# Kernel optimization log

Hardware: AMD Instinct MI355X
Metric: run time of the kernel (lower is better)

## Reference

```python
import jax, jax.numpy as jnp
import numpy as np

B, T, E, D, H = 8, 64, 4, 256, 1024  # batch, num_tokens, num_experts, hidden_dim, ffn_hidden_dim
SPARSITY_WEIGHT = 0.01


def setup_inputs() -> dict:
    key = jax.random.key(0)
    k_x, k_fc1, k_fc2, k_wr, k_br = jax.random.split(key, 5)
    x = jax.random.normal(k_x, (B, T, D), dtype=jnp.float32)
    # xavier_uniform per (t,e) slice: bound = sqrt(6/(fan_in+fan_out))
    a = float(np.sqrt(6.0 / (D + H)))
    fc1 = jax.random.uniform(k_fc1, (T, E, D, H), minval=-a, maxval=a, dtype=jnp.float32)
    b1 = jnp.zeros((T, E, H), dtype=jnp.float32)
    fc2 = jax.random.uniform(k_fc2, (T, E, H, D), minval=-a, maxval=a, dtype=jnp.float32)
    b2 = jnp.zeros((T, E, D), dtype=jnp.float32)
    # per-token routers (nn.Linear default init: U(-1/sqrt(D), 1/sqrt(D)))
    br_bound = float(1.0 / np.sqrt(D))
    Wr = jax.random.uniform(k_wr, (T, E, D), minval=-br_bound, maxval=br_bound, dtype=jnp.float32)
    br = jax.random.uniform(k_br, (T, E), minval=-br_bound, maxval=br_bound, dtype=jnp.float32)
    return {"x": x, "fc1": fc1, "b1": b1, "fc2": fc2, "b2": b2, "Wr": Wr, "br": br}


def reference(x, fc1, b1, fc2, b2, Wr, br):
    # x: [B,T,D]
    # ReLU routing gates per token/expert: [B,T,E]
    gates = jax.nn.relu(jnp.einsum('btd,ted->bte', x, Wr) + br)
    bsz = x.shape[0]
    aux_loss = SPARSITY_WEIGHT * gates.sum() / (bsz * x.shape[1])
    # Expert FFN, batched over (token, expert): hidden [B,T,E,H]
    hidden = jax.nn.gelu(jnp.einsum('btd,tedh->bteh', x, fc1) + b1, approximate=False)
    # dropout rate is 0.0 -> identity
    expert_out = jnp.einsum('bteh,tehd->bted', hidden, fc2) + b2  # [B,T,E,D]
    output = jnp.sum(expert_out * gates[..., None], axis=2)  # [B,T,D]
    return output, aux_loss
```

## Files before the change

kernel.cpp:

```cpp
#include <hip/hip_runtime.h>
#include <hip/hip_bf16.h>

namespace {

constexpr int kB = 8, kT = 64, kE = 4, kD = 256, kH = 1024;
constexpr int kNC = 4;
constexpr int kHc = kH / kNC;

typedef float floatx4 __attribute__((ext_vector_type(4)));

__device__ __forceinline__ float gelu_exact(float v) {
  return 0.5f * v * (1.0f + erff(v * 0.70710678118654752f));
}

__device__ __forceinline__ float4 ntload4(const float4* p) {
  const floatx4 v = __builtin_nontemporal_load(reinterpret_cast<const floatx4*>(p));
  return make_float4(v.x, v.y, v.z, v.w);
}

__global__ __launch_bounds__(256, 4)
void moe_ffn_kernel(const float* __restrict__ x,
                    const float* __restrict__ fc1,
                    const float* __restrict__ b1,
                    const float* __restrict__ fc2,
                    const float* __restrict__ b2,
                    const float* __restrict__ Wr,
                    const float* __restrict__ br,
                    float* __restrict__ out) {
  __shared__ float xs[kB][kD];
  __shared__ float hid[kB][kHc];
  __shared__ float red[kB][kD];
  __shared__ float gates_s[kB];

  const int tid  = threadIdx.x;
  const int bid  = blockIdx.x;
  const int te   = bid >> 2;
  const int c    = bid & 3;
  const int t    = te >> 2;
  const int h0   = c * kHc;
  const int wave = tid >> 6, lane = tid & 63;

  {
    const float4* __restrict__ xsrc = reinterpret_cast<const float4*>(x);
    float4* xdst = reinterpret_cast<float4*>(&xs[0][0]);
#pragma unroll
    for (int i = 0; i < 2; ++i) {
      const int f = i * 256 + tid;
      const int b = f >> 6, d4 = f & 63;
      xdst[f] = xsrc[(size_t)(b * kT + t) * (kD / 4) + d4];
    }
  }
  __syncthreads();

  {
    const float* __restrict__ wr = Wr + (size_t)te * kD;
    const float w0 = wr[lane], w1 = wr[lane + 64], w2 = wr[lane + 128], w3 = wr[lane + 192];
#pragma unroll
    for (int bb = 0; bb < 2; ++bb) {
      const int b = wave * 2 + bb;
      float p = xs[b][lane] * w0 + xs[b][lane + 64] * w1 +
                xs[b][lane + 128] * w2 + xs[b][lane + 192] * w3;
#pragma unroll
      for (int off = 32; off; off >>= 1) p += __shfl_xor(p, off);
      if (lane == 0) {
        const float g = p + br[te];
        gates_s[b] = g > 0.0f ? g : 0.0f;
      }
    }
  }

  float4 acc[kB];
#pragma unroll
  for (int b = 0; b < kB; ++b) acc[b] = make_float4(0.f, 0.f, 0.f, 0.f);
  {
    const float4* __restrict__ wp =
        reinterpret_cast<const float4*>(fc1 + (size_t)te * (kD * kH));
    const int hq = (h0 >> 2) + lane;
    const int d0 = wave * 64;
    for (int dg = 0; dg < 16; ++dg) {
      const int d = d0 + dg * 4;
      const float4 wv0 = wp[(size_t)(d + 0) * (kH / 4) + hq];
      const float4 wv1 = wp[(size_t)(d + 1) * (kH / 4) + hq];
      const float4 wv2 = wp[(size_t)(d + 2) * (kH / 4) + hq];
      const float4 wv3 = wp[(size_t)(d + 3) * (kH / 4) + hq];
#pragma unroll
      for (int b = 0; b < kB; ++b) {
        const float4 xv = *reinterpret_cast<const float4*>(&xs[b][d]);
        acc[b].x = fmaf(xv.x, wv0.x, acc[b].x);
        acc[b].y = fmaf(xv.x, wv0.y, acc[b].y);
        acc[b].z = fmaf(xv.x, wv0.z, acc[b].z);
        acc[b].w = fmaf(xv.x, wv0.w, acc[b].w);
        acc[b].x = fmaf(xv.y, wv1.x, acc[b].x);
        acc[b].y = fmaf(xv.y, wv1.y, acc[b].y);
        acc[b].z = fmaf(xv.y, wv1.z, acc[b].z);
        acc[b].w = fmaf(xv.y, wv1.w, acc[b].w);
        acc[b].x = fmaf(xv.z, wv2.x, acc[b].x);
        acc[b].y = fmaf(xv.z, wv2.y, acc[b].y);
        acc[b].z = fmaf(xv.z, wv2.z, acc[b].z);
        acc[b].w = fmaf(xv.z, wv2.w, acc[b].w);
        acc[b].x = fmaf(xv.w, wv3.x, acc[b].x);
        acc[b].y = fmaf(xv.w, wv3.y, acc[b].y);
        acc[b].z = fmaf(xv.w, wv3.z, acc[b].z);
        acc[b].w = fmaf(xv.w, wv3.w, acc[b].w);
      }
    }
  }
#pragma unroll
  for (int g = 0; g < 4; ++g) {
    if (wave == g) {
#pragma unroll
      for (int b = 0; b < kB; ++b) {
        float4* hp = reinterpret_cast<float4*>(&hid[b][0]) + lane;
        if (g == 0) {
          *hp = acc[b];
        } else {
          float4 v = *hp;
          v.x += acc[b].x; v.y += acc[b].y; v.z += acc[b].z; v.w += acc[b].w;
          *hp = v;
        }
      }
    }
    __syncthreads();
  }
  {
    const float bias = b1[(size_t)te * kH + h0 + tid];
#pragma unroll
    for (int b = 0; b < kB; ++b) hid[b][tid] = gelu_exact(hid[b][tid] + bias);
  }
  __syncthreads();

  float4 acc2[kB];
#pragma unroll
  for (int b = 0; b < kB; ++b) acc2[b] = make_float4(0.f, 0.f, 0.f, 0.f);
  {
    const float4* __restrict__ wp =
        reinterpret_cast<const float4*>(fc2 + (size_t)te * (kH * kD));
    const int hb = wave * 64;
    for (int hg = 0; hg < 16; ++hg) {
      const int hl = hb + hg * 4;
      const int h  = h0 + hl;
      const float4 wv0 = ntload4(wp + (size_t)(h + 0) * (kD / 4) + lane);
      const float4 wv1 = ntload4(wp + (size_t)(h + 1) * (kD / 4) + lane);
      const float4 wv2 = ntload4(wp + (size_t)(h + 2) * (kD / 4) + lane);
      const float4 wv3 = ntload4(wp + (size_t)(h + 3) * (kD / 4) + lane);
#pragma unroll
      for (int b = 0; b < kB; ++b) {
        const float4 hv = *reinterpret_cast<const float4*>(&hid[b][hl]);
        acc2[b].x = fmaf(hv.x, wv0.x, acc2[b].x);
        acc2[b].y = fmaf(hv.x, wv0.y, acc2[b].y);
        acc2[b].z = fmaf(hv.x, wv0.z, acc2[b].z);
        acc2[b].w = fmaf(hv.x, wv0.w, acc2[b].w);
        acc2[b].x = fmaf(hv.y, wv1.x, acc2[b].x);
        acc2[b].y = fmaf(hv.y, wv1.y, acc2[b].y);
        acc2[b].z = fmaf(hv.y, wv1.z, acc2[b].z);
        acc2[b].w = fmaf(hv.y, wv1.w, acc2[b].w);
        acc2[b].x = fmaf(hv.z, wv2.x, acc2[b].x);
        acc2[b].y = fmaf(hv.z, wv2.y, acc2[b].y);
        acc2[b].z = fmaf(hv.z, wv2.z, acc2[b].z);
        acc2[b].w = fmaf(hv.z, wv2.w, acc2[b].w);
        acc2[b].x = fmaf(hv.w, wv3.x, acc2[b].x);
        acc2[b].y = fmaf(hv.w, wv3.y, acc2[b].y);
        acc2[b].z = fmaf(hv.w, wv3.z, acc2[b].z);
        acc2[b].w = fmaf(hv.w, wv3.w, acc2[b].w);
      }
    }
  }
#pragma unroll
  for (int g = 0; g < 4; ++g) {
    if (wave == g) {
#pragma unroll
      for (int b = 0; b < kB; ++b) {
        float4* rp = reinterpret_cast<float4*>(&red[b][0]) + lane;
        if (g == 0) {
          *rp = acc2[b];
        } else {
          float4 v = *rp;
          v.x += acc2[b].x; v.y += acc2[b].y; v.z += acc2[b].z; v.w += acc2[b].w;
          *rp = v;
        }
      }
    }
    __syncthreads();
  }

  {
    const float b2v = (c == 0) ? b2[(size_t)te * kD + tid] : 0.f;
#pragma unroll
    for (int b = 0; b < kB; ++b)
      atomicAdd(&out[((size_t)b * kT + t) * kD + tid], gates_s[b] * (red[b][tid] + b2v));

    if (c == 0 && tid == 0) {
      float gs = 0.f;
#pragma unroll
      for (int b = 0; b < kB; ++b) gs += gates_s[b];
      atomicAdd(&out[(size_t)kB * kT * kD], 0.01f * gs * (1.0f / (kB * kT)));
    }
  }
}

}

extern "C" void kernel_launch(void* const* d_in, const int* in_sizes, int n_in,
                              void* d_out, int out_size, void* d_ws, size_t ws_size,
                              hipStream_t stream) {
  const float* x   = (const float*)d_in[0];
  const float* fc1 = (const float*)d_in[1];
  const float* b1  = (const float*)d_in[2];
  const float* fc2 = (const float*)d_in[3];
  const float* b2  = (const float*)d_in[4];
  const float* Wr  = (const float*)d_in[5];
  const float* br  = (const float*)d_in[6];
  float* out = (float*)d_out;

  (void)hipMemsetAsync(d_out, 0, (size_t)out_size * sizeof(float), stream);

  moe_ffn_kernel<<<dim3(kT * kE * kNC), dim3(256), 0, stream>>>(
      x, fc1, b1, fc2, b2, Wr, br, out);
}
```

Before: 95.89 us.

## Split hidden dim into eight chunks per expert and reuse xs for reduction

Doubles the number of H-chunks per (token, expert) to 2048 blocks, each handling 128 hidden units, to raise parallelism and occupancy (launch bounds raised to 8). The fc1 stage is remapped so half-waves cover different d rows and are combined with a cross-lane shuffle, and fc1 loads become nontemporal. The separate reduction buffer is dropped by reusing xs, which cuts shared memory per block. In exchange, output atomics double and the reduction and sync work per unit of compute grows.

```diff
diff --git a/kernel.cpp b/kernel.cpp
--- a/kernel.cpp
+++ b/kernel.cpp
@@ -4,7 +4,7 @@
 namespace {
 
 constexpr int kB = 8, kT = 64, kE = 4, kD = 256, kH = 1024;
-constexpr int kNC = 4;
+constexpr int kNC = 8;
 constexpr int kHc = kH / kNC;
 
 typedef float floatx4 __attribute__((ext_vector_type(4)));
@@ -18,7 +18,7 @@
   return make_float4(v.x, v.y, v.z, v.w);
 }
 
-__global__ __launch_bounds__(256, 4)
+__global__ __launch_bounds__(256, 8)
 void moe_ffn_kernel(const float* __restrict__ x,
                     const float* __restrict__ fc1,
                     const float* __restrict__ b1,
@@ -29,15 +29,13 @@
                     float* __restrict__ out) {
   __shared__ float xs[kB][kD];
   __shared__ float hid[kB][kHc];
-  __shared__ float red[kB][kD];
   __shared__ float gates_s[kB];
 
   const int tid  = threadIdx.x;
   const int bid  = blockIdx.x;
-  const int te   = bid >> 2;
-  const int c    = bid & 3;
+  const int te   = bid >> 3;
+  const int c    = bid & 7;
   const int t    = te >> 2;
-  const int h0   = c * kHc;
   const int wave = tid >> 6, lane = tid & 63;
 
   {
@@ -69,63 +67,72 @@
     }
   }
 
-  float4 acc[kB];
-#pragma unroll
-  for (int b = 0; b < kB; ++b) acc[b] = make_float4(0.f, 0.f, 0.f, 0.f);
+  const int q = lane & 31, r = lane >> 5;
+  const int hq = c * 32 + q;
+  float4 a[kB];
+#pragma unroll
+  for (int b = 0; b < kB; ++b) a[b] = make_float4(0.f, 0.f, 0.f, 0.f);
   {
     const float4* __restrict__ wp =
         reinterpret_cast<const float4*>(fc1 + (size_t)te * (kD * kH));
-    const int hq = (h0 >> 2) + lane;
     const int d0 = wave * 64;
+#pragma unroll 4
     for (int dg = 0; dg < 16; ++dg) {
-      const int d = d0 + dg * 4;
-      const float4 wv0 = wp[(size_t)(d + 0) * (kH / 4) + hq];
-      const float4 wv1 = wp[(size_t)(d + 1) * (kH / 4) + hq];
-      const float4 wv2 = wp[(size_t)(d + 2) * (kH / 4) + hq];
-      const float4 wv3 = wp[(size_t)(d + 3) * (kH / 4) + hq];
+      const int dbase = d0 + dg * 4;
+      const int row0 = dbase + r;
+      const int row1 = dbase + 2 + r;
+      const float4 wv0 = ntload4(wp + (size_t)row0 * (kH / 4) + hq);
+      const float4 wv1 = ntload4(wp + (size_t)row1 * (kH / 4) + hq);
 #pragma unroll
       for (int b = 0; b < kB; ++b) {
-        const float4 xv = *reinterpret_cast<const float4*>(&xs[b][d]);
-        acc[b].x = fmaf(xv.x, wv0.x, acc[b].x);
-        acc[b].y = fmaf(xv.x, wv0.y, acc[b].y);
-        acc[b].z = fmaf(xv.x, wv0.z, acc[b].z);
-        acc[b].w = fmaf(xv.x, wv0.w, acc[b].w);
-        acc[b].x = fmaf(xv.y, wv1.x, acc[b].x);
-        acc[b].y = fmaf(xv.y, wv1.y, acc[b].y);
-        acc[b].z = fmaf(xv.y, wv1.z, acc[b].z);
-        acc[b].w = fmaf(xv.y, wv1.w, acc[b].w);
-        acc[b].x = fmaf(xv.z, wv2.x, acc[b].x);
-        acc[b].y = fmaf(xv.z, wv2.y, acc[b].y);
-        acc[b].z = fmaf(xv.z, wv2.z, acc[b].z);
-        acc[b].w = fmaf(xv.z, wv2.w, acc[b].w);
-        acc[b].x = fmaf(xv.w, wv3.x, acc[b].x);
-        acc[b].y = fmaf(xv.w, wv3.y, acc[b].y);
-        acc[b].z = fmaf(xv.w, wv3.z, acc[b].z);
-        acc[b].w = fmaf(xv.w, wv3.w, acc[b].w);
-      }
-    }
-  }
-#pragma unroll
-  for (int g = 0; g < 4; ++g) {
-    if (wave == g) {
-#pragma unroll
-      for (int b = 0; b < kB; ++b) {
-        float4* hp = reinterpret_cast<float4*>(&hid[b][0]) + lane;
-        if (g == 0) {
-          *hp = acc[b];
-        } else {
-          float4 v = *hp;
-          v.x += acc[b].x; v.y += acc[b].y; v.z += acc[b].z; v.w += acc[b].w;
-          *hp = v;
+        const float x0 = xs[b][row0];
+        const float x1 = xs[b][row1];
+        a[b].x = fmaf(x0, wv0.x, a[b].x);
+        a[b].y = fmaf(x0, wv0.y, a[b].y);
+        a[b].z = fmaf(x0, wv0.z, a[b].z);
+        a[b].w = fmaf(x0, wv0.w, a[b].w);
+        a[b].x = fmaf(x1, wv1.x, a[b].x);
+        a[b].y = fmaf(x1, wv1.y, a[b].y);
+        a[b].z = fmaf(x1, wv1.z, a[b].z);
+        a[b].w = fmaf(x1, wv1.w, a[b].w);
+      }
+    }
+#pragma unroll
+    for (int b = 0; b < kB; ++b) {
+      a[b].x += __shfl_xor(a[b].x, 32);
+      a[b].y += __shfl_xor(a[b].y, 32);
+      a[b].z += __shfl_xor(a[b].z, 32);
+      a[b].w += __shfl_xor(a[b].w, 32);
+    }
+  }
+  {
+    float4* hidq = reinterpret_cast<float4*>(&hid[0][0]);
+#pragma unroll
+    for (int g = 0; g < 4; ++g) {
+      if (wave == g && lane < 32) {
+#pragma unroll
+        for (int b = 0; b < kB; ++b) {
+          const int idx = b * 32 + q;
+          if (g == 0) {
+            hidq[idx] = a[b];
+          } else {
+            float4 v = hidq[idx];
+            v.x += a[b].x; v.y += a[b].y; v.z += a[b].z; v.w += a[b].w;
+            hidq[idx] = v;
+          }
         }
       }
-    }
-    __syncthreads();
-  }
-  {
-    const float bias = b1[(size_t)te * kH + h0 + tid];
-#pragma unroll
-    for (int b = 0; b < kB; ++b) hid[b][tid] = gelu_exact(hid[b][tid] + bias);
+      __syncthreads();
+    }
+    const int bb = tid >> 5, q2 = tid & 31;
+    float4 v = hidq[bb * 32 + q2];
+    const float4 bias =
+        reinterpret_cast<const float4*>(b1 + (size_t)te * kH + c * kHc)[q2];
+    v.x = gelu_exact(v.x + bias.x);
+    v.y = gelu_exact(v.y + bias.y);
+    v.z = gelu_exact(v.z + bias.z);
+    v.w = gelu_exact(v.w + bias.w);
+    hidq[bb * 32 + q2] = v;
   }
   __syncthreads();
 
@@ -133,16 +140,17 @@
 #pragma unroll
   for (int b = 0; b < kB; ++b) acc2[b] = make_float4(0.f, 0.f, 0.f, 0.f);
   {
-    const float4* __restrict__ wp =
-        reinterpret_cast<const float4*>(fc2 + (size_t)te * (kH * kD));
-    const int hb = wave * 64;
-    for (int hg = 0; hg < 16; ++hg) {
+    const float4* __restrict__ wp2 =
+        reinterpret_cast<const float4*>(fc2 + (size_t)te * (kH * kD)) + lane;
+    const int hb = wave * 32;
+#pragma unroll 2
+    for (int hg = 0; hg < 8; ++hg) {
       const int hl = hb + hg * 4;
-      const int h  = h0 + hl;
-      const float4 wv0 = ntload4(wp + (size_t)(h + 0) * (kD / 4) + lane);
-      const float4 wv1 = ntload4(wp + (size_t)(h + 1) * (kD / 4) + lane);
-      const float4 wv2 = ntload4(wp + (size_t)(h + 2) * (kD / 4) + lane);
-      const float4 wv3 = ntload4(wp + (size_t)(h + 3) * (kD / 4) + lane);
+      const int hrow = c * kHc + hl;
+      const float4 wv0 = ntload4(wp2 + (size_t)(hrow + 0) * (kD / 4));
+      const float4 wv1 = ntload4(wp2 + (size_t)(hrow + 1) * (kD / 4));
+      const float4 wv2 = ntload4(wp2 + (size_t)(hrow + 2) * (kD / 4));
+      const float4 wv3 = ntload4(wp2 + (size_t)(hrow + 3) * (kD / 4));
 #pragma unroll
       for (int b = 0; b < kB; ++b) {
         const float4 hv = *reinterpret_cast<const float4*>(&hid[b][hl]);
@@ -165,29 +173,34 @@
       }
     }
   }
-#pragma unroll
-  for (int g = 0; g < 4; ++g) {
-    if (wave == g) {
-#pragma unroll
-      for (int b = 0; b < kB; ++b) {
-        float4* rp = reinterpret_cast<float4*>(&red[b][0]) + lane;
-        if (g == 0) {
-          *rp = acc2[b];
-        } else {
-          float4 v = *rp;
-          v.x += acc2[b].x; v.y += acc2[b].y; v.z += acc2[b].z; v.w += acc2[b].w;
-          *rp = v;
+  {
+    float4* redq = reinterpret_cast<float4*>(&xs[0][0]);
+#pragma unroll
+    for (int g = 0; g < 4; ++g) {
+      if (wave == g) {
+#pragma unroll
+        for (int b = 0; b < kB; ++b) {
+          const int idx = b * 64 + lane;
+          if (g == 0) {
+            redq[idx] = acc2[b];
+          } else {
+            float4 v = redq[idx];
+            v.x += acc2[b].x; v.y += acc2[b].y; v.z += acc2[b].z; v.w += acc2[b].w;
+            redq[idx] = v;
+          }
         }
       }
-    }
-    __syncthreads();
-  }
-
-  {
+      __syncthreads();
+    }
+  }
+
+  {
+    const float* red = &xs[0][0];
     const float b2v = (c == 0) ? b2[(size_t)te * kD + tid] : 0.f;
 #pragma unroll
     for (int b = 0; b < kB; ++b)
-      atomicAdd(&out[((size_t)b * kT + t) * kD + tid], gates_s[b] * (red[b][tid] + b2v));
+      atomicAdd(&out[((size_t)b * kT + t) * kD + tid],
+                gates_s[b] * (red[b * kD + tid] + b2v));
 
     if (c == 0 && tid == 0) {
       float gs = 0.f;
```

Result: slower. 148.8 us (+55.2%).
